# Optimization experiments

Hardware: AMD Instinct MI355X
Metric: run time of the kernel (lower is better)

## Reference

```python
import jax, jax.numpy as jnp
import numpy as np
import math

B, TT, TS, C, H, L = 8, 256, 512, 512, 8, 10
HD = C // H
TOPK_FRAME = 64
# layer schedule mirrors MultimodalTransformer.forward tower order:
# 4 stimulus cross-attn (kv=frames, topk), 2 causal self-attn, 2 history cross-attn, 2 causal self-attn
# kv_source: 0=frames, 1=self, 2=id_prev
SCHED = [(0, False, TOPK_FRAME)] * 4 + [(1, True, None)] * 2 + [(2, False, None)] * 2 + [(1, True, None)] * 2


def setup_inputs() -> dict:
    key = jax.random.key(0)
    ks = jax.random.split(key, 4)
    kws = jax.random.split(ks[3], 6)
    w = lambda k, s: jax.random.normal(k, s, jnp.float32) * 0.02
    return {
        "id_x": jax.random.normal(ks[0], (B, TT, C), jnp.float32),
        "id_prev": jax.random.normal(ks[1], (B, TT, C), jnp.float32),
        "frames": jax.random.normal(ks[2], (B, TS, C), jnp.float32),
        "Wq": w(kws[0], (L, C, C)), "bq": jnp.zeros((L, C), jnp.float32),
        "Wk": w(kws[1], (L, C, C)), "bk": jnp.zeros((L, C), jnp.float32),
        "Wv": w(kws[2], (L, C, C)), "bv": jnp.zeros((L, C), jnp.float32),
        "Wo": w(kws[3], (L, C, C)), "bo": jnp.zeros((L, C), jnp.float32),
        "W1": w(kws[4], (L, C, 4 * C)), "b1": jnp.zeros((L, 4 * C), jnp.float32),
        "W2": w(kws[5], (L, 4 * C, C)), "b2": jnp.zeros((L, C), jnp.float32),
        "ln1_g": jnp.ones((L, C), jnp.float32), "ln1_b": jnp.zeros((L, C), jnp.float32),
        "ln2_g": jnp.ones((L, C), jnp.float32), "ln2_b": jnp.zeros((L, C), jnp.float32),
        "lnf_g": jnp.ones((L, C), jnp.float32), "lnf_b": jnp.zeros((L, C), jnp.float32),
    }


def _ln(x, g, b):
    mu = x.mean(-1, keepdims=True)
    var = ((x - mu) ** 2).mean(-1, keepdims=True)
    return (x - mu) * jax.lax.rsqrt(var + 1e-5) * g + b


def _block(x, kv, causal, topk, p):
    # Block.forward: x = x + attn(ln1(x), kv, kv, mask); x = x + mlp(ln2(x)); return ln_f(x)
    Wq, bq, Wk, bk, Wv, bv, Wo, bo, W1, b1, W2, b2, l1g, l1b, l2g, l2b, lfg, lfb = p
    Bx, Tt, Cx = x.shape
    Ts = kv.shape[1]
    h = _ln(x, l1g, l1b)
    q = (h @ Wq + bq).reshape(Bx, Tt, H, HD).transpose(0, 2, 1, 3)   # [B,H,Tt,HD]
    k = (kv @ Wk + bk).reshape(Bx, Ts, H, HD).transpose(0, 2, 1, 3)  # [B,H,Ts,HD]
    v = (kv @ Wv + bv).reshape(Bx, Ts, H, HD).transpose(0, 2, 1, 3)
    att = jnp.einsum('bhqd,bhkd->bhqk', q, k) * (1.0 / math.sqrt(HD))
    if causal:
        m = jnp.tril(jnp.ones((Tt, Ts), dtype=bool))
        att = jnp.where(m, att, -jnp.inf)
    if topk is not None and topk < Ts:
        top = jax.lax.top_k(att, topk)[0]           # [B,H,Tt,topk]
        att = jnp.where(att < top[..., -1:], -jnp.inf, att)
    w_att = jax.nn.softmax(att, axis=-1)
    y = jnp.einsum('bhqk,bhkd->bhqd', w_att, v).transpose(0, 2, 1, 3).reshape(Bx, Tt, Cx)
    x = x + y @ Wo + bo
    h2 = _ln(x, l2g, l2b)
    x = x + jax.nn.gelu(h2 @ W1 + b1, approximate=False) @ W2 + b2
    return _ln(x, lfg, lfb)


def _forward(id_x, id_prev, frames, Wq, bq, Wk, bk, Wv, bv, Wo, bo, W1, b1, W2, b2,
             ln1_g, ln1_b, ln2_g, ln2_b, lnf_g, lnf_b):
    x = id_x
    for i, (src, causal, topk) in enumerate(SCHED):
        kv = (frames, x, id_prev)[src]
        p = (Wq[i], bq[i], Wk[i], bk[i], Wv[i], bv[i], Wo[i], bo[i],
             W1[i], b1[i], W2[i], b2[i],
             ln1_g[i], ln1_b[i], ln2_g[i], ln2_b[i], lnf_g[i], lnf_b[i])
        x = _block(x, kv, causal, topk, p)
    return x


def reference(id_x, id_prev, frames, Wq, bq, Wk, bk, Wv, bv, Wo, bo, W1, b1, W2, b2,
              ln1_g, ln1_b, ln2_g, ln2_b, lnf_g, lnf_b):
    return _forward(id_x, id_prev, frames, Wq, bq, Wk, bk, Wv, bv, Wo, bo, W1, b1, W2, b2,
                    ln1_g, ln1_b, ln2_g, ln2_b, lnf_g, lnf_b)
```

## Files before the change

kernel.cpp:

```cpp
#include <hip/hip_runtime.h>
#include <math.h>

#define CC 512
#define NH 8
#define HD 64
#define TT 256

typedef __attribute__((ext_vector_type(8))) short short8v;
typedef __attribute__((ext_vector_type(4))) float f32x4;

__device__ inline unsigned short bfc(float f) {
  unsigned u = __float_as_uint(f);
  return (unsigned short)((u + 0x7fffu + ((u >> 16) & 1u)) >> 16);
}
__device__ inline float b2f(unsigned short s) {
  return __uint_as_float((unsigned)s << 16);
}
__device__ inline void gld16(const void* g, void* l) {
  __builtin_amdgcn_global_load_lds(
      (const __attribute__((address_space(1))) unsigned int*)g,
      (__attribute__((address_space(3))) unsigned int*)l, 16, 0, 0);
}

__global__ __launch_bounds__(256) void prep_k(const float* __restrict__ id_x,
    const float* __restrict__ frames, const float* __restrict__ id_prev,
    float* __restrict__ x, unsigned short* __restrict__ fb,
    unsigned short* __restrict__ pb) {
  int i = blockIdx.x * 256 + threadIdx.x;
  if (i < 262144) {
    ((float4*)x)[i] = ((const float4*)id_x)[i];
  } else if (i < 786432) {
    int j = i - 262144;
    float4 f = ((const float4*)frames)[j];
    ushort4 o; o.x = bfc(f.x); o.y = bfc(f.y); o.z = bfc(f.z); o.w = bfc(f.w);
    ((ushort4*)fb)[j] = o;
  } else {
    int j = i - 786432;
    float4 f = ((const float4*)id_prev)[j];
    ushort4 o; o.x = bfc(f.x); o.y = bfc(f.y); o.z = bfc(f.z); o.w = bfc(f.w);
    ((ushort4*)pb)[j] = o;
  }
}

__global__ __launch_bounds__(256) void ln_bf(const float* __restrict__ in,
    unsigned short* __restrict__ out, const float* __restrict__ g, const float* __restrict__ b) {
  int row = (blockIdx.x << 2) + (threadIdx.x >> 6), lane = threadIdx.x & 63;
  const float* r = in + (size_t)row * CC;
  float4 v0 = *(const float4*)(r + (lane << 2));
  float4 v1 = *(const float4*)(r + 256 + (lane << 2));
  float s = v0.x + v0.y + v0.z + v0.w + v1.x + v1.y + v1.z + v1.w;
  #pragma unroll
  for (int o = 32; o; o >>= 1) s += __shfl_xor(s, o);
  float mu = s * (1.0f / CC);
  float d0x = v0.x - mu, d0y = v0.y - mu, d0z = v0.z - mu, d0w = v0.w - mu;
  float d1x = v1.x - mu, d1y = v1.y - mu, d1z = v1.z - mu, d1w = v1.w - mu;
  float sq = d0x*d0x + d0y*d0y + d0z*d0z + d0w*d0w + d1x*d1x + d1y*d1y + d1z*d1z + d1w*d1w;
  #pragma unroll
  for (int o = 32; o; o >>= 1) sq += __shfl_xor(sq, o);
  float inv = rsqrtf(sq * (1.0f / CC) + 1e-5f);
  float4 g0 = *(const float4*)(g + (lane << 2)), g1 = *(const float4*)(g + 256 + (lane << 2));
  float4 b0 = *(const float4*)(b + (lane << 2)), b1 = *(const float4*)(b + 256 + (lane << 2));
  ushort4 o0, o1;
  o0.x = bfc(d0x*inv*g0.x + b0.x); o0.y = bfc(d0y*inv*g0.y + b0.y);
  o0.z = bfc(d0z*inv*g0.z + b0.z); o0.w = bfc(d0w*inv*g0.w + b0.w);
  o1.x = bfc(d1x*inv*g1.x + b1.x); o1.y = bfc(d1y*inv*g1.y + b1.y);
  o1.z = bfc(d1z*inv*g1.z + b1.z); o1.w = bfc(d1w*inv*g1.w + b1.w);
  *(ushort4*)(out + (size_t)row * CC + (lane << 2)) = o0;
  *(ushort4*)(out + (size_t)row * CC + 256 + (lane << 2)) = o1;
}

__global__ __launch_bounds__(256) void ln_final(const float* __restrict__ in,
    float* __restrict__ out, const float* __restrict__ g, const float* __restrict__ b) {
  int row = (blockIdx.x << 2) + (threadIdx.x >> 6), lane = threadIdx.x & 63;
  const float* r = in + (size_t)row * CC;
  float4 v0 = *(const float4*)(r + (lane << 2));
  float4 v1 = *(const float4*)(r + 256 + (lane << 2));
  float s = v0.x + v0.y + v0.z + v0.w + v1.x + v1.y + v1.z + v1.w;
  #pragma unroll
  for (int o = 32; o; o >>= 1) s += __shfl_xor(s, o);
  float mu = s * (1.0f / CC);
  float d0x = v0.x - mu, d0y = v0.y - mu, d0z = v0.z - mu, d0w = v0.w - mu;
  float d1x = v1.x - mu, d1y = v1.y - mu, d1z = v1.z - mu, d1w = v1.w - mu;
  float sq = d0x*d0x + d0y*d0y + d0z*d0z + d0w*d0w + d1x*d1x + d1y*d1y + d1z*d1z + d1w*d1w;
  #pragma unroll
  for (int o = 32; o; o >>= 1) sq += __shfl_xor(sq, o);
  float inv = rsqrtf(sq * (1.0f / CC) + 1e-5f);
  float4 g0 = *(const float4*)(g + (lane << 2)), g1 = *(const float4*)(g + 256 + (lane << 2));
  float4 b0 = *(const float4*)(b + (lane << 2)), b1 = *(const float4*)(b + 256 + (lane << 2));
  float4 o0, o1;
  o0.x = d0x*inv*g0.x + b0.x; o0.y = d0y*inv*g0.y + b0.y;
  o0.z = d0z*inv*g0.z + b0.z; o0.w = d0w*inv*g0.w + b0.w;
  o1.x = d1x*inv*g1.x + b1.x; o1.y = d1y*inv*g1.y + b1.y;
  o1.z = d1z*inv*g1.z + b1.z; o1.w = d1w*inv*g1.w + b1.w;
  *(float4*)(out + (size_t)row * CC + (lane << 2)) = o0;
  *(float4*)(out + (size_t)row * CC + 256 + (lane << 2)) = o1;
}

__global__ __launch_bounds__(256) void ln_chain(const float* __restrict__ in,
    float* __restrict__ xout, unsigned short* __restrict__ xb,
    const float* __restrict__ gf, const float* __restrict__ bf,
    const float* __restrict__ g1, const float* __restrict__ b1,
    unsigned short* __restrict__ hout) {
  int row = (blockIdx.x << 2) + (threadIdx.x >> 6), lane = threadIdx.x & 63;
  const float* r = in + (size_t)row * CC;
  float4 v0 = *(const float4*)(r + (lane << 2));
  float4 v1 = *(const float4*)(r + 256 + (lane << 2));
  float s = v0.x + v0.y + v0.z + v0.w + v1.x + v1.y + v1.z + v1.w;
  #pragma unroll
  for (int o = 32; o; o >>= 1) s += __shfl_xor(s, o);
  float mu = s * (1.0f / CC);
  float d0x = v0.x - mu, d0y = v0.y - mu, d0z = v0.z - mu, d0w = v0.w - mu;
  float d1x = v1.x - mu, d1y = v1.y - mu, d1z = v1.z - mu, d1w = v1.w - mu;
  float sq = d0x*d0x + d0y*d0y + d0z*d0z + d0w*d0w + d1x*d1x + d1y*d1y + d1z*d1z + d1w*d1w;
  #pragma unroll
  for (int o = 32; o; o >>= 1) sq += __shfl_xor(sq, o);
  float inv = rsqrtf(sq * (1.0f / CC) + 1e-5f);
  float4 g0 = *(const float4*)(gf + (lane << 2)), g1v = *(const float4*)(gf + 256 + (lane << 2));
  float4 b0 = *(const float4*)(bf + (lane << 2)), b1v = *(const float4*)(bf + 256 + (lane << 2));
  float4 x0, x1;
  x0.x = d0x*inv*g0.x + b0.x; x0.y = d0y*inv*g0.y + b0.y;
  x0.z = d0z*inv*g0.z + b0.z; x0.w = d0w*inv*g0.w + b0.w;
  x1.x = d1x*inv*g1v.x + b1v.x; x1.y = d1y*inv*g1v.y + b1v.y;
  x1.z = d1z*inv*g1v.z + b1v.z; x1.w = d1w*inv*g1v.w + b1v.w;
  *(float4*)(xout + (size_t)row * CC + (lane << 2)) = x0;
  *(float4*)(xout + (size_t)row * CC + 256 + (lane << 2)) = x1;
  ushort4 xb0, xb1;
  xb0.x = bfc(x0.x); xb0.y = bfc(x0.y); xb0.z = bfc(x0.z); xb0.w = bfc(x0.w);
  xb1.x = bfc(x1.x); xb1.y = bfc(x1.y); xb1.z = bfc(x1.z); xb1.w = bfc(x1.w);
  *(ushort4*)(xb + (size_t)row * CC + (lane << 2)) = xb0;
  *(ushort4*)(xb + (size_t)row * CC + 256 + (lane << 2)) = xb1;
  float s2 = x0.x + x0.y + x0.z + x0.w + x1.x + x1.y + x1.z + x1.w;
  #pragma unroll
  for (int o = 32; o; o >>= 1) s2 += __shfl_xor(s2, o);
  float mu2 = s2 * (1.0f / CC);
  float e0x = x0.x - mu2, e0y = x0.y - mu2, e0z = x0.z - mu2, e0w = x0.w - mu2;
  float e1x = x1.x - mu2, e1y = x1.y - mu2, e1z = x1.z - mu2, e1w = x1.w - mu2;
  float sq2 = e0x*e0x + e0y*e0y + e0z*e0z + e0w*e0w + e1x*e1x + e1y*e1y + e1z*e1z + e1w*e1w;
  #pragma unroll
  for (int o = 32; o; o >>= 1) sq2 += __shfl_xor(sq2, o);
  float inv2 = rsqrtf(sq2 * (1.0f / CC) + 1e-5f);
  float4 h0 = *(const float4*)(g1 + (lane << 2)), h1 = *(const float4*)(g1 + 256 + (lane << 2));
  float4 c0 = *(const float4*)(b1 + (lane << 2)), c1 = *(const float4*)(b1 + 256 + (lane << 2));
  ushort4 ho0, ho1;
  ho0.x = bfc(e0x*inv2*h0.x + c0.x); ho0.y = bfc(e0y*inv2*h0.y + c0.y);
  ho0.z = bfc(e0z*inv2*h0.z + c0.z); ho0.w = bfc(e0w*inv2*h0.w + c0.w);
  ho1.x = bfc(e1x*inv2*h1.x + c1.x); ho1.y = bfc(e1y*inv2*h1.y + c1.y);
  ho1.z = bfc(e1z*inv2*h1.z + c1.z); ho1.w = bfc(e1w*inv2*h1.w + c1.w);
  *(ushort4*)(hout + (size_t)row * CC + (lane << 2)) = ho0;
  *(ushort4*)(hout + (size_t)row * CC + 256 + (lane << 2)) = ho1;
}

__global__ __launch_bounds__(256) void transpose_w(
    const float* __restrict__ Wq, const float* __restrict__ Wk,
    const float* __restrict__ Wv, const float* __restrict__ Wo,
    const float* __restrict__ W1, const float* __restrict__ W2,
    int layer_base, unsigned short* __restrict__ wT) {
  int lz = blockIdx.x / 768;
  int layer = layer_base + lz;
  int bid = blockIdx.x - lz * 768;
  unsigned short* wTl = wT + (size_t)lz * 3145728;
  const float* src; unsigned short* dst; int R, Cn, tile, lgc;
  if (bid < 256) {
    int seg = bid >> 6; tile = bid & 63; R = 512; Cn = 512; lgc = 3;
    const float* s4[4] = {Wq, Wk, Wv, Wo};
    src = s4[seg] + (size_t)layer * 262144;
    dst = wTl + (size_t)seg * 262144;
  } else if (bid < 512) {
    tile = bid - 256; R = 512; Cn = 2048; lgc = 5;
    src = W1 + (size_t)layer * 1048576; dst = wTl + 1048576;
  } else {
    tile = bid - 512; R = 2048; Cn = 512; lgc = 3;
    src = W2 + (size_t)layer * 1048576; dst = wTl + 2097152;
  }
  int trb = tile >> lgc, tcb = tile & ((1 << lgc) - 1);
  __shared__ float tl[64][65];
  int t = threadIdx.x;
  int r = t >> 2, c0 = (t & 3) << 4;
  const float* sp = src + (size_t)(trb * 64 + r) * Cn + tcb * 64 + c0;
  #pragma unroll
  for (int j = 0; j < 4; j++) {
    float4 fv = *(const float4*)(sp + (j << 2));
    tl[r][c0 + (j << 2)]     = fv.x; tl[r][c0 + (j << 2) + 1] = fv.y;
    tl[r][c0 + (j << 2) + 2] = fv.z; tl[r][c0 + (j << 2) + 3] = fv.w;
  }
  __syncthreads();
  unsigned short* dp = dst + (size_t)(tcb * 64 + r) * R + trb * 64 + c0;
  #pragma unroll
  for (int j = 0; j < 4; j++) {
    ushort4 ov;
    ov.x = bfc(tl[c0 + (j << 2)][r]);     ov.y = bfc(tl[c0 + (j << 2) + 1][r]);
    ov.z = bfc(tl[c0 + (j << 2) + 2][r]); ov.w = bfc(tl[c0 + (j << 2) + 3][r]);
    *(ushort4*)(dp + (j << 2)) = ov;
  }
}

template<int BM, int GELU, int RES, int OUTBF, int BIAS2, int QSC>
__global__ __launch_bounds__(256) void gemm_bf(
    const unsigned short* __restrict__ A, const unsigned short* __restrict__ WT,
    const float* __restrict__ bias, const float* __restrict__ bias2,
    void* __restrict__ outp, const float* __restrict__ res, int M, int N, int K) {
  __shared__ __align__(16) unsigned short As[2][BM * 64];
  __shared__ __align__(16) unsigned short Bs[2][64 * 64];
  const int tid = threadIdx.x, lane = tid & 63, wid = tid >> 6;
  const int bm = blockIdx.y * BM, bn = blockIdx.x << 6;
  const int wm = (wid >> 1) * (BM / 2), wn = (wid & 1) << 5;
  constexpr int MF = BM / 32;
  f32x4 acc[MF][2] = {};
  const int fr = lane & 15, fq = lane >> 4;
  const int srow_a = tid >> 3, sgc = tid & 7;
  const int sgcs = sgc ^ (srow_a & 7);

  auto stage = [&](int buf, int k0) {
    #pragma unroll
    for (int i = 0; i < BM / 32; i++) {
      int row = srow_a + (i << 5);
      int gcs = sgc ^ (row & 7);
      gld16(A + (size_t)(bm + row) * K + k0 + (gcs << 3),
            (char*)As[buf] + (i << 12) + (wid << 10));
    }
    #pragma unroll
    for (int i = 0; i < 2; i++) {
      int row = srow_a + (i << 5);
      int gcs = sgc ^ (row & 7);
      gld16(WT + (size_t)(bn + row) * K + k0 + (gcs << 3),
            (char*)Bs[buf] + (i << 12) + (wid << 10));
    }
  };

  stage(0, 0);
  __syncthreads();
  int cur = 0;
  for (int k0 = 0; k0 < K; k0 += 64) {
    if (k0 + 64 < K) stage(cur ^ 1, k0 + 64);
    short8v af[MF][2], bf2[2][2];
    #pragma unroll
    for (int mf = 0; mf < MF; mf++)
      #pragma unroll
      for (int ks = 0; ks < 2; ks++) {
        int r = wm + mf * 16 + fr;
        int c = (ks << 2) + fq;
        af[mf][ks] = *(const short8v*)((const char*)As[cur] + ((((r << 7) + (c << 4))) ^ ((r & 7) << 4)));
      }
    #pragma unroll
    for (int nf = 0; nf < 2; nf++)
      #pragma unroll
      for (int ks = 0; ks < 2; ks++) {
        int r = wn + nf * 16 + fr;
        int c = (ks << 2) + fq;
        bf2[nf][ks] = *(const short8v*)((const char*)Bs[cur] + ((((r << 7) + (c << 4))) ^ ((r & 7) << 4)));
      }
    #pragma unroll
    for (int mf = 0; mf < MF; mf++)
      #pragma unroll
      for (int nf = 0; nf < 2; nf++) {
        acc[mf][nf] = __builtin_amdgcn_mfma_f32_16x16x32_bf16(af[mf][0], bf2[nf][0], acc[mf][nf], 0, 0, 0);
        acc[mf][nf] = __builtin_amdgcn_mfma_f32_16x16x32_bf16(af[mf][1], bf2[nf][1], acc[mf][nf], 0, 0, 0);
      }
    __syncthreads();
    cur ^= 1;
  }
  #pragma unroll
  for (int mf = 0; mf < MF; mf++)
    #pragma unroll
    for (int nf = 0; nf < 2; nf++) {
      int col = bn + wn + nf * 16 + fr;
      float bia = (BIAS2 && col >= 512) ? bias2[col - 512] : bias[col];
      #pragma unroll
      for (int rr = 0; rr < 4; rr++) {
        int row = bm + wm + mf * 16 + fq * 4 + rr;
        float vv = acc[mf][nf][rr] + bia;
        if (GELU) vv = 0.5f * vv * (1.0f + erff(vv * 0.70710678118654752f));
        if (RES)  vv += res[(size_t)row * N + col];
        if (QSC)  vv *= 0.125f;
        if (OUTBF) ((unsigned short*)outp)[(size_t)row * N + col] = bfc(vv);
        else       ((float*)outp)[(size_t)row * N + col] = vv;
      }
    }
}

template<int CAUSAL, int TOPK, int TSK>
__global__ __launch_bounds__(512, 4) void attn_m(
    const unsigned short* __restrict__ qb, const unsigned short* __restrict__ kv,
    unsigned short* __restrict__ yb) {
  constexpr int NT = TSK / 64;
  constexpr int NKC = TSK / 128;
  constexpr int SST = TSK + 8;
  __shared__ float S[8 * SST];
  __shared__ __align__(16) unsigned short Ks[128 * 64];
  __shared__ __align__(16) unsigned short Qs[16 * 64];
  __shared__ float swt[TOPK ? 8 : 1][TOPK ? 128 : 1];
  __shared__ unsigned short kidx[TOPK ? 8 : 1][TOPK ? 128 : 1];
  int tid = threadIdx.x, lane = tid & 63, wid = tid >> 6;
  int bid = blockIdx.x;
  int swz = ((bid & 7) << 8) | (bid >> 3);
  int b = swz >> 8, h = (swz >> 5) & 7, q0 = (swz & 31) << 3;
  if (tid < 64) {
    int row = tid >> 3, sp = tid & 7;
    gld16(qb + (size_t)((b << 8) + q0 + row) * CC + (h << 6) + ((sp ^ (row & 7)) << 3),
          (char*)Qs);
  } else if (tid < 128) {
    short8v z = {0, 0, 0, 0, 0, 0, 0, 0};
    *(short8v*)((char*)Qs + (tid << 4)) = z;
  }
  __syncthreads();
  short8v aF[2];
  {
    int r = lane & 15, kq2 = lane >> 4;
    #pragma unroll
    for (int kc2 = 0; kc2 < 2; kc2++)
      aF[kc2] = *(const short8v*)((const char*)Qs +
                 (((r << 7) + (kc2 << 6) + (kq2 << 4)) ^ ((r & 7) << 4)));
  }
  int nte = NKC;
  if (CAUSAL) { int ub = (q0 + 8 + 127) >> 7; nte = ub < NKC ? ub : NKC; }
  const unsigned short* kgb = kv + (size_t)b * TSK * 1024 + (h << 6);
  for (int t = 0; t < nte; t++) {
    __syncthreads();
    #pragma unroll
    for (int j = 0; j < 2; j++) {
      int s = (wid << 7) + (j << 6) + lane;
      int row = s >> 3, sp = s & 7;
      gld16(kgb + (size_t)((t << 7) + row) * 1024 + ((sp ^ (row & 7)) << 3),
            (char*)Ks + (wid << 11) + (j << 10));
    }
    __syncthreads();
    int kq2 = lane >> 4;
    f32x4 acc = {};
    int key16 = (wid << 4) + (lane & 15);
    #pragma unroll
    for (int kc2 = 0; kc2 < 2; kc2++) {
      short8v bF = *(const short8v*)((const char*)Ks +
                    (((key16 << 7) + (kc2 << 6) + (kq2 << 4)) ^ ((key16 & 7) << 4)));
      acc = __builtin_amdgcn_mfma_f32_16x16x32_bf16(aF[kc2], bF, acc, 0, 0, 0);
    }
    if (kq2 < 2) {
      int col = (t << 7) + key16;
      #pragma unroll
      for (int r = 0; r < 4; r++)
        S[(kq2 * 4 + r) * SST + col] = acc[r];
    }
  }
  __syncthreads();
  int row = wid;
  int qi = q0 + row;
  int jmax = CAUSAL ? (qi + 1) : TSK;
  const unsigned short* vgb = kv + (size_t)b * TSK * 1024 + 512 + (h << 6) + lane;
  float sc[NT];
  float lmax = -3.0e38f;
  #pragma unroll
  for (int tt = 0; tt < NT; tt++) {
    int key = lane + (tt << 6);
    float v = (!CAUSAL || key < jmax) ? S[row * SST + key] : -3.0e38f;
    sc[tt] = v;
    lmax = fmaxf(lmax, v);
  }
  float mx = lmax;
  #pragma unroll
  for (int o = 32; o; o >>= 1) mx = fmaxf(mx, __shfl_xor(mx, o));
  float oacc = 0.f;
  if (TOPK) {
    unsigned key[NT];
    #pragma unroll
    for (int tt = 0; tt < NT; tt++) {
      unsigned u = __float_as_uint(sc[tt]);
      key[tt] = (u & 0x80000000u) ? ~u : (u | 0x80000000u);
    }
    unsigned prefix = 0u;
    for (int bit = 31; bit >= 0; bit--) {
      unsigned cand = prefix | (1u << bit);
      int cnt = 0;
      #pragma unroll
      for (int tt = 0; tt < NT; tt++)
        cnt += __popcll(__ballot(key[tt] >= cand));
      if (cnt >= 64) {
        prefix = cand;
        if (cnt == 64) break;
      }
    }
    float wvv[NT];
    float psum = 0.f;
    int basec = 0;
    #pragma unroll
    for (int tt = 0; tt < NT; tt++) {
      bool keep = key[tt] >= prefix;
      float wv = keep ? exp2f((sc[tt] - mx) * 1.4426950408889634f) : 0.f;
      wvv[tt] = wv;
      psum += wv;
      unsigned long long mask = __ballot(keep);
      if (keep) {
        int pos = basec + (int)__popcll(mask & ((1ull << lane) - 1ull));
        if (pos < 128) {
          kidx[row][pos] = (unsigned short)(lane + (tt << 6));
          swt[row][pos] = wv;
        }
      }
      basec += (int)__popcll(mask);
    }
    #pragma unroll
    for (int o = 32; o; o >>= 1) psum += __shfl_xor(psum, o);
    float inv = 1.0f / psum;
    int nk = basec;
    if (nk <= 128) {
      float a0 = 0.f, a1 = 0.f, a2 = 0.f, a3 = 0.f;
      int i = 0;
      for (; i + 3 < nk; i += 4) {
        a0 += swt[row][i]     * b2f(vgb[(size_t)kidx[row][i] * 1024]);
        a1 += swt[row][i + 1] * b2f(vgb[(size_t)kidx[row][i + 1] * 1024]);
        a2 += swt[row][i + 2] * b2f(vgb[(size_t)kidx[row][i + 2] * 1024]);
        a3 += swt[row][i + 3] * b2f(vgb[(size_t)kidx[row][i + 3] * 1024]);
      }
      for (; i < nk; i++) a0 += swt[row][i] * b2f(vgb[(size_t)kidx[row][i] * 1024]);
      oacc = (a0 + a1 + a2 + a3) * inv;
    } else {
      #pragma unroll
      for (int tt = 0; tt < NT; tt++)
        S[row * SST + lane + (tt << 6)] = wvv[tt];
      float a0 = 0.f, a1 = 0.f;
      for (int j = 0; j + 1 < TSK; j += 2) {
        a0 += S[row * SST + j]     * b2f(vgb[(size_t)j * 1024]);
        a1 += S[row * SST + j + 1] * b2f(vgb[(size_t)(j + 1) * 1024]);
      }
      oacc = (a0 + a1) * inv;
    }
  } else {
    float psum = 0.f;
    #pragma unroll
    for (int tt = 0; tt < NT; tt++) {
      int keyj = lane + (tt << 6);
      float wv = (keyj < jmax) ? exp2f((sc[tt] - mx) * 1.4426950408889634f) : 0.f;
      S[row * SST + keyj] = wv;
      psum += wv;
    }
    #pragma unroll
    for (int o = 32; o; o >>= 1) psum += __shfl_xor(psum, o);
    float inv = 1.0f / psum;
    float a0 = 0.f, a1 = 0.f, a2 = 0.f, a3 = 0.f;
    int j = 0;
    for (; j + 3 < jmax; j += 4) {
      a0 += S[row * SST + j]     * b2f(vgb[(size_t)j * 1024]);
      a1 += S[row * SST + j + 1] * b2f(vgb[(size_t)(j + 1) * 1024]);
      a2 += S[row * SST + j + 2] * b2f(vgb[(size_t)(j + 2) * 1024]);
      a3 += S[row * SST + j + 3] * b2f(vgb[(size_t)(j + 3) * 1024]);
    }
    for (; j < jmax; j++) a0 += S[row * SST + j] * b2f(vgb[(size_t)j * 1024]);
    oacc = (a0 + a1 + a2 + a3) * inv;
  }
  yb[(size_t)((b << 8) + qi) * CC + (h << 6) + lane] = bfc(oacc);
}

extern "C" void kernel_launch(void* const* d_in, const int* in_sizes, int n_in,
                              void* d_out, int out_size, void* d_ws, size_t ws_size,
                              hipStream_t stream) {
  const float* id_x    = (const float*)d_in[0];
  const float* id_prev = (const float*)d_in[1];
  const float* frames  = (const float*)d_in[2];
  const float* Wq = (const float*)d_in[3];  const float* bq = (const float*)d_in[4];
  const float* Wk = (const float*)d_in[5];  const float* bk = (const float*)d_in[6];
  const float* Wv = (const float*)d_in[7];  const float* bv = (const float*)d_in[8];
  const float* Wo = (const float*)d_in[9];  const float* bo = (const float*)d_in[10];
  const float* W1 = (const float*)d_in[11]; const float* b1 = (const float*)d_in[12];
  const float* W2 = (const float*)d_in[13]; const float* b2 = (const float*)d_in[14];
  const float* l1g = (const float*)d_in[15]; const float* l1b = (const float*)d_in[16];
  const float* l2g = (const float*)d_in[17]; const float* l2b = (const float*)d_in[18];
  const float* lfg = (const float*)d_in[19]; const float* lfb = (const float*)d_in[20];

  float* x = (float*)d_out;
  char* W  = (char*)d_ws;
  unsigned short* qbuf = (unsigned short*)W;
  unsigned short* kvb  = (unsigned short*)(W + ((size_t)4  << 20));
  unsigned short* m1b  = (unsigned short*)(W + ((size_t)4  << 20));
  unsigned short* hb   = (unsigned short*)(W + ((size_t)12 << 20));
  unsigned short* ybf  = (unsigned short*)(W + ((size_t)14 << 20));
  unsigned short* xb   = (unsigned short*)(W + ((size_t)16 << 20));
  unsigned short* fb   = (unsigned short*)(W + ((size_t)18 << 20));
  unsigned short* pb   = (unsigned short*)(W + ((size_t)22 << 20));
  unsigned short* wT   = (unsigned short*)(W + ((size_t)24 << 20));

  const bool allw = ws_size >= (((size_t)24 << 20) + (size_t)10 * 3145728 * 2);

  prep_k<<<4096, 256, 0, stream>>>(id_x, frames, id_prev, x, fb, pb);
  if (allw)
    transpose_w<<<7680, 256, 0, stream>>>(Wq, Wk, Wv, Wo, W1, W2, 0, wT);

  static const int ssrc[10] = {0, 0, 0, 0, 1, 1, 2, 2, 1, 1};

  for (int i = 0; i < 10; i++) {
    if (!allw)
      transpose_w<<<768, 256, 0, stream>>>(Wq, Wk, Wv, Wo, W1, W2, i, wT);
    unsigned short* wTl = wT + (allw ? (size_t)i * 3145728 : 0);
    unsigned short* wqT = wTl;
    unsigned short* wkvT = wTl + 262144;
    unsigned short* woT = wTl + 786432;
    unsigned short* w1T = wTl + 1048576;
    unsigned short* w2T = wTl + 2097152;

    if (i == 0)
      ln_bf<<<512, 256, 0, stream>>>(x, hb, l1g, l1b);

    gemm_bf<32, 0, 0, 1, 0, 1><<<dim3(8, 64), 256, 0, stream>>>(hb, wqT, bq + i * 512, nullptr, qbuf, nullptr, 2048, 512, 512);

    const unsigned short* kvsrc; int Mkv;
    if (ssrc[i] == 0)      { kvsrc = fb; Mkv = 4096; }
    else if (ssrc[i] == 1) { kvsrc = xb; Mkv = 2048; }
    else                   { kvsrc = pb; Mkv = 2048; }
    if (Mkv == 4096)
      gemm_bf<64, 0, 0, 1, 1, 0><<<dim3(16, 64), 256, 0, stream>>>(kvsrc, wkvT, bk + i * 512, bv + i * 512, kvb, nullptr, 4096, 1024, 512);
    else
      gemm_bf<32, 0, 0, 1, 1, 0><<<dim3(16, 64), 256, 0, stream>>>(kvsrc, wkvT, bk + i * 512, bv + i * 512, kvb, nullptr, 2048, 1024, 512);

    if (ssrc[i] == 0)      attn_m<0, 1, 512><<<2048, 512, 0, stream>>>(qbuf, kvb, ybf);
    else if (ssrc[i] == 1) attn_m<1, 0, 256><<<2048, 512, 0, stream>>>(qbuf, kvb, ybf);
    else                   attn_m<0, 0, 256><<<2048, 512, 0, stream>>>(qbuf, kvb, ybf);

    gemm_bf<32, 0, 1, 0, 0, 0><<<dim3(8, 64), 256, 0, stream>>>(ybf, woT, bo + i * 512, nullptr, x, x, 2048, 512, 512);
    ln_bf<<<512, 256, 0, stream>>>(x, hb, l2g + i * 512, l2b + i * 512);
    gemm_bf<64, 1, 0, 1, 0, 0><<<dim3(32, 32), 256, 0, stream>>>(hb, w1T, b1 + i * 2048, nullptr, m1b, nullptr, 2048, 2048, 512);
    gemm_bf<32, 0, 1, 0, 0, 0><<<dim3(8, 64), 256, 0, stream>>>(m1b, w2T, b2 + i * 512, nullptr, x, x, 2048, 512, 2048);

    if (i < 9)
      ln_chain<<<512, 256, 0, stream>>>(x, x, xb, lfg + i * 512, lfb + i * 512,
                                        l1g + (i + 1) * 512, l1b + (i + 1) * 512, hb);
    else
      ln_final<<<512, 256, 0, stream>>>(x, x, lfg + i * 512, lfb + i * 512);
  }
}
```

Measured before the change: 1.037 ms.

## Fuse Q and KV projections into one launch, retile W1 GEMM and transpose

Adds a gemm_qkv kernel that computes the Q projection and the K/V projection in a single launch, with the first 256 blocks doing Q and the rest doing KV. This removes one kernel launch per layer and lets the two GEMMs share the GPU. The W1 GEMM moves from BM=64 to BM=128 tiles, giving fewer blocks with more reuse per block. The weight transpose switches from 64x64 to 32x32 tiles and launches four times as many blocks. The larger W1 tile raises register and LDS pressure, and the fused QKV kernel always uses 64-row tiles, including for the smaller KV inputs.

Measured after the change: 1.011 ms. 2.5% less time.

```diff
diff --git a/kernel.cpp b/kernel.cpp
--- a/kernel.cpp
+++ b/kernel.cpp
@@ -155,43 +155,36 @@
     const float* __restrict__ Wv, const float* __restrict__ Wo,
     const float* __restrict__ W1, const float* __restrict__ W2,
     int layer_base, unsigned short* __restrict__ wT) {
-  int lz = blockIdx.x / 768;
+  int lz = blockIdx.x / 3072;
   int layer = layer_base + lz;
-  int bid = blockIdx.x - lz * 768;
+  int bid = blockIdx.x - lz * 3072;
   unsigned short* wTl = wT + (size_t)lz * 3145728;
-  const float* src; unsigned short* dst; int R, Cn, tile, lgc;
-  if (bid < 256) {
-    int seg = bid >> 6; tile = bid & 63; R = 512; Cn = 512; lgc = 3;
+  const float* src; unsigned short* dst; int R, Cn, tile, lg;
+  if (bid < 1024) {
+    int seg = bid >> 8; tile = bid & 255; R = 512; Cn = 512; lg = 4;
     const float* s4[4] = {Wq, Wk, Wv, Wo};
     src = s4[seg] + (size_t)layer * 262144;
     dst = wTl + (size_t)seg * 262144;
-  } else if (bid < 512) {
-    tile = bid - 256; R = 512; Cn = 2048; lgc = 5;
+  } else if (bid < 2048) {
+    tile = bid - 1024; R = 512; Cn = 2048; lg = 6;
     src = W1 + (size_t)layer * 1048576; dst = wTl + 1048576;
   } else {
-    tile = bid - 512; R = 2048; Cn = 512; lgc = 3;
+    tile = bid - 2048; R = 2048; Cn = 512; lg = 4;
     src = W2 + (size_t)layer * 1048576; dst = wTl + 2097152;
   }
-  int trb = tile >> lgc, tcb = tile & ((1 << lgc) - 1);
-  __shared__ float tl[64][65];
+  int trb = tile >> lg, tcb = tile & ((1 << lg) - 1);
+  __shared__ float tl[32][33];
   int t = threadIdx.x;
-  int r = t >> 2, c0 = (t & 3) << 4;
-  const float* sp = src + (size_t)(trb * 64 + r) * Cn + tcb * 64 + c0;
-  #pragma unroll
-  for (int j = 0; j < 4; j++) {
-    float4 fv = *(const float4*)(sp + (j << 2));
-    tl[r][c0 + (j << 2)]     = fv.x; tl[r][c0 + (j << 2) + 1] = fv.y;
-    tl[r][c0 + (j << 2) + 2] = fv.z; tl[r][c0 + (j << 2) + 3] = fv.w;
-  }
+  int r = t >> 3, c4 = (t & 7) << 2;
+  const float* sp = src + (size_t)(trb * 32 + r) * Cn + tcb * 32 + c4;
+  float4 fv = *(const float4*)sp;
+  tl[r][c4] = fv.x; tl[r][c4 + 1] = fv.y; tl[r][c4 + 2] = fv.z; tl[r][c4 + 3] = fv.w;
   __syncthreads();
-  unsigned short* dp = dst + (size_t)(tcb * 64 + r) * R + trb * 64 + c0;
-  #pragma unroll
-  for (int j = 0; j < 4; j++) {
-    ushort4 ov;
-    ov.x = bfc(tl[c0 + (j << 2)][r]);     ov.y = bfc(tl[c0 + (j << 2) + 1][r]);
-    ov.z = bfc(tl[c0 + (j << 2) + 2][r]); ov.w = bfc(tl[c0 + (j << 2) + 3][r]);
-    *(ushort4*)(dp + (j << 2)) = ov;
-  }
+  unsigned short* dp = dst + (size_t)(tcb * 32 + r) * R + trb * 32 + c4;
+  ushort4 ov;
+  ov.x = bfc(tl[c4][r]); ov.y = bfc(tl[c4 + 1][r]);
+  ov.z = bfc(tl[c4 + 2][r]); ov.w = bfc(tl[c4 + 3][r]);
+  *(ushort4*)dp = ov;
 }
 
 template<int BM, int GELU, int RES, int OUTBF, int BIAS2, int QSC>
@@ -208,7 +201,6 @@
   f32x4 acc[MF][2] = {};
   const int fr = lane & 15, fq = lane >> 4;
   const int srow_a = tid >> 3, sgc = tid & 7;
-  const int sgcs = sgc ^ (srow_a & 7);
 
   auto stage = [&](int buf, int k0) {
     #pragma unroll
@@ -274,6 +266,86 @@
         if (QSC)  vv *= 0.125f;
         if (OUTBF) ((unsigned short*)outp)[(size_t)row * N + col] = bfc(vv);
         else       ((float*)outp)[(size_t)row * N + col] = vv;
+      }
+    }
+}
+
+__global__ __launch_bounds__(256) void gemm_qkv(
+    const unsigned short* __restrict__ hb, const unsigned short* __restrict__ wqT,
+    const float* __restrict__ bq,
+    const unsigned short* __restrict__ kvA, const unsigned short* __restrict__ wkvT,
+    const float* __restrict__ bk, const float* __restrict__ bv,
+    unsigned short* __restrict__ qout, unsigned short* __restrict__ kvout) {
+  const int tid = threadIdx.x, lane = tid & 63, wid = tid >> 6;
+  int bid = blockIdx.x;
+  const unsigned short *A, *WT;
+  const float *bias, *bias2;
+  unsigned short* outp;
+  int bm, bn, N;
+  bool isq = bid < 256;
+  if (isq) {
+    A = hb; WT = wqT; bias = bq; bias2 = bq; outp = qout; N = 512;
+    bm = (bid >> 3) << 6; bn = (bid & 7) << 6;
+  } else {
+    int t = bid - 256;
+    A = kvA; WT = wkvT; bias = bk; bias2 = bv; outp = kvout; N = 1024;
+    bm = (t >> 4) << 6; bn = (t & 15) << 6;
+  }
+  __shared__ __align__(16) unsigned short As[2][64 * 64];
+  __shared__ __align__(16) unsigned short Bs[2][64 * 64];
+  const int wm = (wid >> 1) << 5, wn = (wid & 1) << 5;
+  f32x4 acc[2][2] = {};
+  const int fr = lane & 15, fq = lane >> 4;
+  const int srow_a = tid >> 3, sgc = tid & 7;
+  auto stage = [&](int buf, int k0) {
+    #pragma unroll
+    for (int i = 0; i < 2; i++) {
+      int row = srow_a + (i << 5);
+      int gcs = sgc ^ (row & 7);
+      gld16(A + (size_t)(bm + row) * 512 + k0 + (gcs << 3),
+            (char*)As[buf] + (i << 12) + (wid << 10));
+      gld16(WT + (size_t)(bn + row) * 512 + k0 + (gcs << 3),
+            (char*)Bs[buf] + (i << 12) + (wid << 10));
+    }
+  };
+  stage(0, 0);
+  __syncthreads();
+  int cur = 0;
+  for (int k0 = 0; k0 < 512; k0 += 64) {
+    if (k0 + 64 < 512) stage(cur ^ 1, k0 + 64);
+    short8v af[2][2], bf2[2][2];
+    #pragma unroll
+    for (int mf = 0; mf < 2; mf++)
+      #pragma unroll
+      for (int ks = 0; ks < 2; ks++) {
+        int r = wm + mf * 16 + fr;
+        int c = (ks << 2) + fq;
+        af[mf][ks] = *(const short8v*)((const char*)As[cur] + ((((r << 7) + (c << 4))) ^ ((r & 7) << 4)));
+        int r2 = wn + mf * 16 + fr;
+        bf2[mf][ks] = *(const short8v*)((const char*)Bs[cur] + ((((r2 << 7) + (c << 4))) ^ ((r2 & 7) << 4)));
+      }
+    #pragma unroll
+    for (int mf = 0; mf < 2; mf++)
+      #pragma unroll
+      for (int nf = 0; nf < 2; nf++) {
+        acc[mf][nf] = __builtin_amdgcn_mfma_f32_16x16x32_bf16(af[mf][0], bf2[nf][0], acc[mf][nf], 0, 0, 0);
+        acc[mf][nf] = __builtin_amdgcn_mfma_f32_16x16x32_bf16(af[mf][1], bf2[nf][1], acc[mf][nf], 0, 0, 0);
+      }
+    __syncthreads();
+    cur ^= 1;
+  }
+  #pragma unroll
+  for (int mf = 0; mf < 2; mf++)
+    #pragma unroll
+    for (int nf = 0; nf < 2; nf++) {
+      int col = bn + wn + nf * 16 + fr;
+      float bia = (col >= 512) ? bias2[col - 512] : bias[col];
+      #pragma unroll
+      for (int rr = 0; rr < 4; rr++) {
+        int row = bm + wm + mf * 16 + fq * 4 + rr;
+        float vv = acc[mf][nf][rr] + bia;
+        if (isq) vv *= 0.125f;
+        outp[(size_t)row * N + col] = bfc(vv);
       }
     }
 }
@@ -480,13 +552,13 @@
 
   prep_k<<<4096, 256, 0, stream>>>(id_x, frames, id_prev, x, fb, pb);
   if (allw)
-    transpose_w<<<7680, 256, 0, stream>>>(Wq, Wk, Wv, Wo, W1, W2, 0, wT);
+    transpose_w<<<30720, 256, 0, stream>>>(Wq, Wk, Wv, Wo, W1, W2, 0, wT);
 
   static const int ssrc[10] = {0, 0, 0, 0, 1, 1, 2, 2, 1, 1};
 
   for (int i = 0; i < 10; i++) {
     if (!allw)
-      transpose_w<<<768, 256, 0, stream>>>(Wq, Wk, Wv, Wo, W1, W2, i, wT);
+      transpose_w<<<3072, 256, 0, stream>>>(Wq, Wk, Wv, Wo, W1, W2, i, wT);
     unsigned short* wTl = wT + (allw ? (size_t)i * 3145728 : 0);
     unsigned short* wqT = wTl;
     unsigned short* wkvT = wTl + 262144;
@@ -497,16 +569,12 @@
     if (i == 0)
       ln_bf<<<512, 256, 0, stream>>>(x, hb, l1g, l1b);
 
-    gemm_bf<32, 0, 0, 1, 0, 1><<<dim3(8, 64), 256, 0, stream>>>(hb, wqT, bq + i * 512, nullptr, qbuf, nullptr, 2048, 512, 512);
-
     const unsigned short* kvsrc; int Mkv;
     if (ssrc[i] == 0)      { kvsrc = fb; Mkv = 4096; }
     else if (ssrc[i] == 1) { kvsrc = xb; Mkv = 2048; }
     else                   { kvsrc = pb; Mkv = 2048; }
-    if (Mkv == 4096)
-      gemm_bf<64, 0, 0, 1, 1, 0><<<dim3(16, 64), 256, 0, stream>>>(kvsrc, wkvT, bk + i * 512, bv + i * 512, kvb, nullptr, 4096, 1024, 512);
-    else
-      gemm_bf<32, 0, 0, 1, 1, 0><<<dim3(16, 64), 256, 0, stream>>>(kvsrc, wkvT, bk + i * 512, bv + i * 512, kvb, nullptr, 2048, 1024, 512);
+    gemm_qkv<<<256 + (Mkv / 64) * 16, 256, 0, stream>>>(
+        hb, wqT, bq + i * 512, kvsrc, wkvT, bk + i * 512, bv + i * 512, qbuf, kvb);
 
     if (ssrc[i] == 0)      attn_m<0, 1, 512><<<2048, 512, 0, stream>>>(qbuf, kvb, ybf);
     else if (ssrc[i] == 1) attn_m<1, 0, 256><<<2048, 512, 0, stream>>>(qbuf, kvb, ybf);
@@ -514,7 +582,7 @@
 
     gemm_bf<32, 0, 1, 0, 0, 0><<<dim3(8, 64), 256, 0, stream>>>(ybf, woT, bo + i * 512, nullptr, x, x, 2048, 512, 512);
     ln_bf<<<512, 256, 0, stream>>>(x, hb, l2g + i * 512, l2b + i * 512);
-    gemm_bf<64, 1, 0, 1, 0, 0><<<dim3(32, 32), 256, 0, stream>>>(hb, w1T, b1 + i * 2048, nullptr, m1b, nullptr, 2048, 2048, 512);
+    gemm_bf<128, 1, 0, 1, 0, 0><<<dim3(32, 16), 256, 0, stream>>>(hb, w1T, b1 + i * 2048, nullptr, m1b, nullptr, 2048, 2048, 512);
     gemm_bf<32, 0, 1, 0, 0, 0><<<dim3(8, 64), 256, 0, stream>>>(m1b, w2T, b2 + i * 512, nullptr, x, x, 2048, 512, 2048);
 
     if (i < 9)
```
